# Performance work log

Measured on AMD Instinct MI355X. Metric: run time of the kernel, lower is better.

## Reference

```python
import jax, jax.numpy as jnp
import numpy as np

N_NODES = 100000


def gcn_conv(x, edge_index, W, b):
    """PyG-style GCNConv: add self-loops, symmetric deg^-1/2 normalization,
    linear transform, scatter-add aggregation."""
    n = x.shape[0]
    x = x @ W  # [N, F_out]
    # add self-loops (fixed shape -> jit friendly)
    loops = jnp.arange(n, dtype=edge_index.dtype)
    src = jnp.concatenate([edge_index[0], loops])
    dst = jnp.concatenate([edge_index[1], loops])
    # degree computed on target nodes (col), incl. self-loops
    deg = jax.ops.segment_sum(jnp.ones_like(dst, dtype=x.dtype), dst, num_segments=n)
    deg_inv_sqrt = jnp.where(deg > 0, jax.lax.rsqrt(deg), 0.0)
    norm = deg_inv_sqrt[src] * deg_inv_sqrt[dst]  # [E+N]
    msgs = x[src] * norm[:, None]  # gather + scale
    out = jax.ops.segment_sum(msgs, dst, num_segments=n)  # scatter-add
    return out + b


def setup_inputs() -> dict:
    key = jax.random.key(0)
    k1, k2, k3, k4 = jax.random.split(key, 4)
    x = jax.random.normal(k1, (N_NODES, 1), dtype=jnp.float32)
    edge_index = jax.random.randint(k2, (2, 3200000), 0, N_NODES, dtype=jnp.int64)
    W1 = jax.random.normal(k3, (1, 16), dtype=jnp.float32) * (1.0 / np.sqrt(1))
    b1 = jnp.zeros((16,), dtype=jnp.float32)
    W2 = jax.random.normal(k4, (16, 2), dtype=jnp.float32) * (1.0 / np.sqrt(16))
    b2 = jnp.zeros((2,), dtype=jnp.float32)
    return {"x": x, "edge_index": edge_index, "W1": W1, "b1": b1, "W2": W2, "b2": b2}


def reference(x, edge_index, W1, b1, W2, b2):
    h = gcn_conv(x, edge_index, W1, b1)
    h = jax.nn.relu(h)
    out = gcn_conv(h, edge_index, W2, b2)
    return out
```

## Files before the change

### kernel.cpp

```cpp
#include <hip/hip_runtime.h>

#define N_NODES 100000
#define NP 100096
#define N_EDGES 3200000
#define NB 782
#define NBP 1024
#define NHR 400
#define EPB (N_EDGES / NHR)
#define RS 10368
#define BSB 512
#define CAP 6144
#define CAPO 5120
#define CSRS 5120
#define SENT 128u

typedef unsigned char u8;

__global__ __launch_bounds__(BSB) void k_bin3(const int* __restrict__ src,
                                              const int* __restrict__ dst,
                                              unsigned* __restrict__ binned,
                                              unsigned* __restrict__ runinfoT) {
    __shared__ int hist[NBP];
    __shared__ int scanv[NBP];
    __shared__ int sh[BSB];
    __shared__ alignas(16) unsigned stage[RS];
    int t = threadIdx.x, blk = blockIdx.x;
    for (int i = t; i < NBP; i += BSB) hist[i] = 0;
    for (int i = t; i < RS; i += BSB) stage[i] = SENT;
    __syncthreads();
    int base = blk * EPB;
    for (int i = t * 4; i < EPB; i += BSB * 4) {
        int4 d = *(const int4*)(dst + base + i);
        atomicAdd(&hist[d.x >> 7], 1);
        atomicAdd(&hist[d.y >> 7], 1);
        atomicAdd(&hist[d.z >> 7], 1);
        atomicAdd(&hist[d.w >> 7], 1);
    }
    __syncthreads();
    int c0 = hist[2 * t], c1 = hist[2 * t + 1];
    int p0 = (c0 + 3) & ~3, p1 = (c1 + 3) & ~3;
    int v = p0 + p1;
    sh[t] = v;
    __syncthreads();
    for (int off = 1; off < BSB; off <<= 1) {
        int u = (t >= off) ? sh[t - off] : 0;
        __syncthreads();
        sh[t] += u;
        __syncthreads();
    }
    int excl = sh[t] - v;
    scanv[2 * t] = excl;
    scanv[2 * t + 1] = excl + p0;
    __syncthreads();
    for (int b = t; b < NB; b += BSB)
        runinfoT[(size_t)b * NHR + blk] =
            (unsigned)scanv[b] | ((unsigned)((hist[b] + 3) >> 2) << 16);
    __syncthreads();
    for (int i = t * 4; i < EPB; i += BSB * 4) {
        int4 s4 = *(const int4*)(src + base + i);
        int4 d4 = *(const int4*)(dst + base + i);
        int p;
        p = atomicAdd(&scanv[d4.x >> 7], 1);
        stage[p] = ((unsigned)s4.x << 8) | (unsigned)(d4.x & 127);
        p = atomicAdd(&scanv[d4.y >> 7], 1);
        stage[p] = ((unsigned)s4.y << 8) | (unsigned)(d4.y & 127);
        p = atomicAdd(&scanv[d4.z >> 7], 1);
        stage[p] = ((unsigned)s4.z << 8) | (unsigned)(d4.z & 127);
        p = atomicAdd(&scanv[d4.w >> 7], 1);
        stage[p] = ((unsigned)s4.w << 8) | (unsigned)(d4.w & 127);
    }
    __syncthreads();
    for (int i = t * 4; i < RS; i += BSB * 4)
        *(int4*)(binned + (size_t)blk * RS + i) = *(const int4*)(stage + i);
}

__global__ __launch_bounds__(256) void k_regroup(
        const unsigned* __restrict__ binned, const unsigned* __restrict__ runinfoT,
        const float* __restrict__ x, unsigned* __restrict__ csr,
        int* __restrict__ startv, int* __restrict__ lenv,
        float* __restrict__ dinv, float* __restrict__ s) {
    __shared__ unsigned rinfo[NHR];
    __shared__ int pref[512];
    __shared__ int sh[256];
    __shared__ alignas(16) unsigned stage[CAP];
    __shared__ unsigned outA[CAPO];
    __shared__ int cnt[128];
    __shared__ int excl[128];
    __shared__ int cur[128];
    int t = threadIdx.x, b = blockIdx.x;
    for (int r = t; r < NHR; r += 256) rinfo[r] = runinfoT[(size_t)b * NHR + r];
    if (t < 128) cnt[t] = 0;
    __syncthreads();
    int v0 = (2 * t < NHR) ? 4 * (int)(rinfo[2 * t] >> 16) : 0;
    int v1 = (2 * t + 1 < NHR) ? 4 * (int)(rinfo[2 * t + 1] >> 16) : 0;
    int vv = v0 + v1;
    sh[t] = vv;
    __syncthreads();
    for (int off = 1; off < 256; off <<= 1) {
        int u = (t >= off) ? sh[t - off] : 0;
        __syncthreads();
        sh[t] += u;
        __syncthreads();
    }
    int ex = sh[t] - vv;
    pref[2 * t] = ex;
    pref[2 * t + 1] = ex + v0;
    __syncthreads();
    int padTot = sh[255];
    int g = t >> 2, lane = t & 3;
    for (int r = g; r < NHR; r += 64) {
        unsigned ri = rinfo[r];
        int off = (int)(ri & 0xFFFFu), nq = (int)(ri >> 16);
        int bs = pref[r];
        if (bs + 4 * nq > CAP) continue;
        const uint4* p = (const uint4*)(binned + (size_t)r * RS + off);
        for (int j = lane; j < nq; j += 4) {
            uint4 w = p[j];
            *(uint4*)(&stage[bs + 4 * j]) = make_uint4(w.x, w.y, w.z, w.w);
        }
    }
    __syncthreads();
    for (int i = t; i < padTot; i += 256) {
        unsigned w = stage[i];
        if ((w & 255u) != 128u) atomicAdd(&cnt[w & 127], 1);
    }
    __syncthreads();
    if (t < 128) sh[t] = cnt[t];
    __syncthreads();
    for (int off = 1; off < 128; off <<= 1) {
        int u = (t >= off && t < 128) ? sh[t - off] : 0;
        __syncthreads();
        if (t < 128) sh[t] += u;
        __syncthreads();
    }
    if (t < 128) {
        excl[t] = sh[t] - cnt[t];
        cur[t] = sh[t] - cnt[t];
    }
    __syncthreads();
    for (int i = t; i < padTot; i += 256) {
        unsigned w = stage[i];
        if ((w & 255u) != 128u) {
            int pos = atomicAdd(&cur[w & 127], 1);
            if (pos < CAPO) outA[pos] = w >> 8;
        }
    }
    __syncthreads();
    int fillTot = excl[127] + cnt[127];
    if (fillTot > CAPO) fillTot = CAPO;
    for (int i = t; i < fillTot; i += 256)
        csr[(size_t)b * CSRS + i] = outA[i];
    if (t < 128) {
        int node = b * 128 + t;
        if (node < N_NODES) {
            int d = cnt[t];
            float di = rsqrtf((float)(d + 1));
            dinv[node] = di;
            s[node] = di * x[node];
            startv[node] = b * CSRS + excl[t];
            lenv[node] = d;
        }
    }
}

__global__ __launch_bounds__(256) void k_s1c(const unsigned* __restrict__ csr,
                                             const int* __restrict__ startv,
                                             const int* __restrict__ lenv,
                                             const float* __restrict__ dinv,
                                             const float* __restrict__ s,
                                             const float* __restrict__ W1,
                                             const float* __restrict__ b1,
                                             const float* __restrict__ W2,
                                             float2* __restrict__ z) {
    int v = blockIdx.x * 256 + threadIdx.x;
    if (v >= N_NODES) return;
    int st = startv[v], n = lenv[v];
    const unsigned* p = csr + st;
    float a0 = 0.f, a1 = 0.f, a2 = 0.f, a3 = 0.f;
    int j = 0;
    for (; j + 4 <= n; j += 4) {
        unsigned c0 = p[j], c1 = p[j + 1], c2 = p[j + 2], c3 = p[j + 3];
        float f0 = s[c0], f1 = s[c1], f2 = s[c2], f3 = s[c3];
        a0 += f0;
        a1 += f1;
        a2 += f2;
        a3 += f3;
    }
    float acc = (a0 + a1) + (a2 + a3);
    for (; j < n; ++j) acc += s[p[j]];
    float di = dinv[v];
    float a = di * (acc + s[v]);
    float z0 = 0.f, z1 = 0.f;
#pragma unroll
    for (int f = 0; f < 16; ++f) {
        float h = fmaxf(a * W1[f] + b1[f], 0.f);
        z0 += h * W2[2 * f + 0];
        z1 += h * W2[2 * f + 1];
    }
    z[v] = make_float2(di * z0, di * z1);
}

__global__ __launch_bounds__(256) void k_s2c(const unsigned* __restrict__ csr,
                                             const int* __restrict__ startv,
                                             const int* __restrict__ lenv,
                                             const float* __restrict__ dinv,
                                             const float2* __restrict__ z,
                                             const float* __restrict__ b2,
                                             float2* __restrict__ out) {
    int v = blockIdx.x * 256 + threadIdx.x;
    if (v >= N_NODES) return;
    int st = startv[v], n = lenv[v];
    const unsigned* p = csr + st;
    float x0 = 0.f, y0 = 0.f, x1 = 0.f, y1 = 0.f;
    float x2 = 0.f, y2 = 0.f, x3 = 0.f, y3 = 0.f;
    int j = 0;
    for (; j + 4 <= n; j += 4) {
        unsigned c0 = p[j], c1 = p[j + 1], c2 = p[j + 2], c3 = p[j + 3];
        float2 f0 = z[c0], f1 = z[c1], f2 = z[c2], f3 = z[c3];
        x0 += f0.x;
        y0 += f0.y;
        x1 += f1.x;
        y1 += f1.y;
        x2 += f2.x;
        y2 += f2.y;
        x3 += f3.x;
        y3 += f3.y;
    }
    float ax = (x0 + x1) + (x2 + x3);
    float ay = (y0 + y1) + (y2 + y3);
    for (; j < n; ++j) {
        float2 f = z[p[j]];
        ax += f.x;
        ay += f.y;
    }
    float2 zz = z[v];
    float di = dinv[v];
    out[v] = make_float2(di * (ax + zz.x) + b2[0], di * (ay + zz.y) + b2[1]);
}

__global__ void f_deg(const int* __restrict__ dst, int* __restrict__ deg) {
    int i = blockIdx.x * blockDim.x + threadIdx.x;
    if (i < N_EDGES) atomicAdd(&deg[dst[i]], 1);
}
__global__ void f_node1(const float* __restrict__ x, const int* __restrict__ deg,
                        float* __restrict__ dinv, float* __restrict__ s) {
    int v = blockIdx.x * blockDim.x + threadIdx.x;
    if (v < N_NODES) {
        float di = rsqrtf((float)(deg[v] + 1));
        dinv[v] = di;
        s[v] = di * x[v];
    }
}
__global__ void f_scatter1(const int* __restrict__ src, const int* __restrict__ dst,
                           const float* __restrict__ s, float* __restrict__ agg1) {
    int i = blockIdx.x * blockDim.x + threadIdx.x;
    if (i < N_EDGES) atomicAdd(&agg1[dst[i]], s[src[i]]);
}
__global__ void f_node2(const float* __restrict__ dinv, const float* __restrict__ s,
                        const float* __restrict__ agg1, const float* __restrict__ W1,
                        const float* __restrict__ b1, const float* __restrict__ W2,
                        float2* __restrict__ z) {
    int v = blockIdx.x * blockDim.x + threadIdx.x;
    if (v < N_NODES) {
        float di = dinv[v];
        float a = di * (agg1[v] + s[v]);
        float z0 = 0.f, z1 = 0.f;
#pragma unroll
        for (int f = 0; f < 16; ++f) {
            float h = fmaxf(a * W1[f] + b1[f], 0.f);
            z0 += h * W2[2 * f + 0];
            z1 += h * W2[2 * f + 1];
        }
        z[v] = make_float2(di * z0, di * z1);
    }
}
__global__ void f_scatter2(const int* __restrict__ src, const int* __restrict__ dst,
                           const float2* __restrict__ z, float* __restrict__ agg2) {
    int i = blockIdx.x * blockDim.x + threadIdx.x;
    if (i < N_EDGES) {
        float2 zz = z[src[i]];
        int d = dst[i];
        atomicAdd(&agg2[2 * d + 0], zz.x);
        atomicAdd(&agg2[2 * d + 1], zz.y);
    }
}
__global__ void f_out(const float* __restrict__ dinv, const float2* __restrict__ z,
                      const float2* __restrict__ agg2, const float* __restrict__ b2,
                      float2* __restrict__ out) {
    int v = blockIdx.x * blockDim.x + threadIdx.x;
    if (v < N_NODES) {
        float di = dinv[v];
        float2 a = agg2[v], zz = z[v];
        out[v] = make_float2(di * (a.x + zz.x) + b2[0], di * (a.y + zz.y) + b2[1]);
    }
}

extern "C" void kernel_launch(void* const* d_in, const int* in_sizes, int n_in,
                              void* d_out, int out_size, void* d_ws, size_t ws_size,
                              hipStream_t stream) {
    const float* x  = (const float*)d_in[0];
    const int* eidx = (const int*)d_in[1];
    const float* W1 = (const float*)d_in[2];
    const float* b1 = (const float*)d_in[3];
    const float* W2 = (const float*)d_in[4];
    const float* b2 = (const float*)d_in[5];
    float* out = (float*)d_out;

    const int n = N_NODES;
    const int* src = eidx;
    const int* dst = eidx + N_EDGES;

    size_t oRun   = 0;
    size_t oBin   = oRun + (size_t)NB * NHR;
    size_t oCsr   = oBin + (size_t)NHR * RS;
    size_t oStart = oCsr + (size_t)NB * CSRS;
    size_t oLen   = oStart + NP;
    size_t oDinv  = oLen + NP;
    size_t oS     = oDinv + NP;
    size_t oZ     = oS + NP;
    size_t need   = (oZ + 2 * NP) * sizeof(int);

    if (ws_size >= need) {
        int* wsI = (int*)d_ws;
        unsigned* runinfoT = (unsigned*)(wsI + oRun);
        unsigned* binned   = (unsigned*)(wsI + oBin);
        unsigned* csr      = (unsigned*)(wsI + oCsr);
        int* startv = wsI + oStart;
        int* lenv   = wsI + oLen;
        float* dinv = (float*)(wsI + oDinv);
        float* s    = (float*)(wsI + oS);
        float2* z   = (float2*)(wsI + oZ);

        k_bin3<<<NHR, BSB, 0, stream>>>(src, dst, binned, runinfoT);
        k_regroup<<<NB, 256, 0, stream>>>(binned, runinfoT, x, csr, startv, lenv,
                                          dinv, s);
        k_s1c<<<NP / 256, 256, 0, stream>>>(csr, startv, lenv, dinv, s, W1, b1,
                                            W2, z);
        k_s2c<<<NP / 256, 256, 0, stream>>>(csr, startv, lenv, dinv, z, b2,
                                            (float2*)out);
    } else {
        float* ws = (float*)d_ws;
        int* deg    = (int*)ws;
        float* agg1 = ws + n;
        float* agg2 = ws + 2 * n;
        float* dinv = ws + 4 * n;
        float* s    = ws + 5 * n;
        float* z    = ws + 6 * n;
        (void)hipMemsetAsync(d_ws, 0, (size_t)(4 * n) * sizeof(float), stream);
        const int gridE = (N_EDGES + 255) / 256;
        const int gridN = (n + 255) / 256;
        f_deg<<<gridE, 256, 0, stream>>>(dst, deg);
        f_node1<<<gridN, 256, 0, stream>>>(x, deg, dinv, s);
        f_scatter1<<<gridE, 256, 0, stream>>>(src, dst, s, agg1);
        f_node2<<<gridN, 256, 0, stream>>>(dinv, s, agg1, W1, b1, W2, (float2*)z);
        f_scatter2<<<gridE, 256, 0, stream>>>(src, dst, (const float2*)z, agg2);
        f_out<<<gridN, 256, 0, stream>>>(dinv, (const float2*)z, (const float2*)agg2,
                                         b2, (float2*)out);
    }
}
```

Measured before the change: 87.20 us.

## Pad CSR rows to 4 and gather with 4 lanes per node using uint4 loads

```diff
diff --git a/kernel.cpp b/kernel.cpp
--- a/kernel.cpp
+++ b/kernel.cpp
@@ -85,11 +85,12 @@
     __shared__ alignas(16) unsigned stage[CAP];
     __shared__ unsigned outA[CAPO];
     __shared__ int cnt[128];
-    __shared__ int excl[128];
+    __shared__ int excl4[128];
     __shared__ int cur[128];
     int t = threadIdx.x, b = blockIdx.x;
     for (int r = t; r < NHR; r += 256) rinfo[r] = runinfoT[(size_t)b * NHR + r];
     if (t < 128) cnt[t] = 0;
+    for (int i = t; i < CAPO; i += 256) outA[i] = 0xFFFFFFFFu;
     __syncthreads();
     int v0 = (2 * t < NHR) ? 4 * (int)(rinfo[2 * t] >> 16) : 0;
     int v1 = (2 * t + 1 < NHR) ? 4 * (int)(rinfo[2 * t + 1] >> 16) : 0;
@@ -125,7 +126,7 @@
         if ((w & 255u) != 128u) atomicAdd(&cnt[w & 127], 1);
     }
     __syncthreads();
-    if (t < 128) sh[t] = cnt[t];
+    if (t < 128) sh[t] = (cnt[t] + 3) & ~3;
     __syncthreads();
     for (int off = 1; off < 128; off <<= 1) {
         int u = (t >= off && t < 128) ? sh[t - off] : 0;
@@ -134,8 +135,9 @@
         __syncthreads();
     }
     if (t < 128) {
-        excl[t] = sh[t] - cnt[t];
-        cur[t] = sh[t] - cnt[t];
+        int pc = (cnt[t] + 3) & ~3;
+        excl4[t] = sh[t] - pc;
+        cur[t] = sh[t] - pc;
     }
     __syncthreads();
     for (int i = t; i < padTot; i += 256) {
@@ -146,7 +148,7 @@
         }
     }
     __syncthreads();
-    int fillTot = excl[127] + cnt[127];
+    int fillTot = excl4[127] + ((cnt[127] + 3) & ~3);
     if (fillTot > CAPO) fillTot = CAPO;
     for (int i = t; i < fillTot; i += 256)
         csr[(size_t)b * CSRS + i] = outA[i];
@@ -157,7 +159,7 @@
             float di = rsqrtf((float)(d + 1));
             dinv[node] = di;
             s[node] = di * x[node];
-            startv[node] = b * CSRS + excl[t];
+            startv[node] = b * CSRS + excl4[t];
             lenv[node] = d;
         }
     }
@@ -172,32 +174,36 @@
                                              const float* __restrict__ b1,
                                              const float* __restrict__ W2,
                                              float2* __restrict__ z) {
-    int v = blockIdx.x * 256 + threadIdx.x;
+    int t = threadIdx.x;
+    int v = blockIdx.x * 64 + (t >> 2);
+    int lane = t & 3;
     if (v >= N_NODES) return;
-    int st = startv[v], n = lenv[v];
-    const unsigned* p = csr + st;
-    float a0 = 0.f, a1 = 0.f, a2 = 0.f, a3 = 0.f;
-    int j = 0;
-    for (; j + 4 <= n; j += 4) {
-        unsigned c0 = p[j], c1 = p[j + 1], c2 = p[j + 2], c3 = p[j + 3];
-        float f0 = s[c0], f1 = s[c1], f2 = s[c2], f3 = s[c3];
-        a0 += f0;
-        a1 += f1;
-        a2 += f2;
-        a3 += f3;
-    }
-    float acc = (a0 + a1) + (a2 + a3);
-    for (; j < n; ++j) acc += s[p[j]];
-    float di = dinv[v];
-    float a = di * (acc + s[v]);
-    float z0 = 0.f, z1 = 0.f;
+    int st = startv[v], d = lenv[v];
+    int nq = (d + 3) >> 2;
+    const uint4* p = (const uint4*)(csr + st);
+    float acc = 0.f;
+    for (int j = lane; j < nq; j += 4) {
+        uint4 w = p[j];
+        float f0 = (w.x < N_NODES) ? s[w.x] : 0.f;
+        float f1 = (w.y < N_NODES) ? s[w.y] : 0.f;
+        float f2 = (w.z < N_NODES) ? s[w.z] : 0.f;
+        float f3 = (w.w < N_NODES) ? s[w.w] : 0.f;
+        acc += (f0 + f1) + (f2 + f3);
+    }
+    acc += __shfl_xor(acc, 1);
+    acc += __shfl_xor(acc, 2);
+    if (lane == 0) {
+        float di = dinv[v];
+        float a = di * (acc + s[v]);
+        float z0 = 0.f, z1 = 0.f;
 #pragma unroll
-    for (int f = 0; f < 16; ++f) {
-        float h = fmaxf(a * W1[f] + b1[f], 0.f);
-        z0 += h * W2[2 * f + 0];
-        z1 += h * W2[2 * f + 1];
-    }
-    z[v] = make_float2(di * z0, di * z1);
+        for (int f = 0; f < 16; ++f) {
+            float h = fmaxf(a * W1[f] + b1[f], 0.f);
+            z0 += h * W2[2 * f + 0];
+            z1 += h * W2[2 * f + 1];
+        }
+        z[v] = make_float2(di * z0, di * z1);
+    }
 }
 
 __global__ __launch_bounds__(256) void k_s2c(const unsigned* __restrict__ csr,
@@ -207,35 +213,30 @@
                                              const float2* __restrict__ z,
                                              const float* __restrict__ b2,
                                              float2* __restrict__ out) {
-    int v = blockIdx.x * 256 + threadIdx.x;
+    int t = threadIdx.x;
+    int v = blockIdx.x * 64 + (t >> 2);
+    int lane = t & 3;
     if (v >= N_NODES) return;
-    int st = startv[v], n = lenv[v];
-    const unsigned* p = csr + st;
-    float x0 = 0.f, y0 = 0.f, x1 = 0.f, y1 = 0.f;
-    float x2 = 0.f, y2 = 0.f, x3 = 0.f, y3 = 0.f;
-    int j = 0;
-    for (; j + 4 <= n; j += 4) {
-        unsigned c0 = p[j], c1 = p[j + 1], c2 = p[j + 2], c3 = p[j + 3];
-        float2 f0 = z[c0], f1 = z[c1], f2 = z[c2], f3 = z[c3];
-        x0 += f0.x;
-        y0 += f0.y;
-        x1 += f1.x;
-        y1 += f1.y;
-        x2 += f2.x;
-        y2 += f2.y;
-        x3 += f3.x;
-        y3 += f3.y;
-    }
-    float ax = (x0 + x1) + (x2 + x3);
-    float ay = (y0 + y1) + (y2 + y3);
-    for (; j < n; ++j) {
-        float2 f = z[p[j]];
-        ax += f.x;
-        ay += f.y;
-    }
-    float2 zz = z[v];
-    float di = dinv[v];
-    out[v] = make_float2(di * (ax + zz.x) + b2[0], di * (ay + zz.y) + b2[1]);
+    int st = startv[v], d = lenv[v];
+    int nq = (d + 3) >> 2;
+    const uint4* p = (const uint4*)(csr + st);
+    float ax = 0.f, ay = 0.f;
+    for (int j = lane; j < nq; j += 4) {
+        uint4 w = p[j];
+        if (w.x < N_NODES) { float2 f = z[w.x]; ax += f.x; ay += f.y; }
+        if (w.y < N_NODES) { float2 f = z[w.y]; ax += f.x; ay += f.y; }
+        if (w.z < N_NODES) { float2 f = z[w.z]; ax += f.x; ay += f.y; }
+        if (w.w < N_NODES) { float2 f = z[w.w]; ax += f.x; ay += f.y; }
+    }
+    ax += __shfl_xor(ax, 1);
+    ax += __shfl_xor(ax, 2);
+    ay += __shfl_xor(ay, 1);
+    ay += __shfl_xor(ay, 2);
+    if (lane == 0) {
+        float2 zz = z[v];
+        float di = dinv[v];
+        out[v] = make_float2(di * (ax + zz.x) + b2[0], di * (ay + zz.y) + b2[1]);
+    }
 }
 
 __global__ void f_deg(const int* __restrict__ dst, int* __restrict__ deg) {
@@ -331,13 +332,14 @@
         float* s    = (float*)(wsI + oS);
         float2* z   = (float2*)(wsI + oZ);
 
+        const int gridS = (N_NODES + 63) / 64;
         k_bin3<<<NHR, BSB, 0, stream>>>(src, dst, binned, runinfoT);
         k_regroup<<<NB, 256, 0, stream>>>(binned, runinfoT, x, csr, startv, lenv,
                                           dinv, s);
-        k_s1c<<<NP / 256, 256, 0, stream>>>(csr, startv, lenv, dinv, s, W1, b1,
-                                            W2, z);
-        k_s2c<<<NP / 256, 256, 0, stream>>>(csr, startv, lenv, dinv, z, b2,
-                                            (float2*)out);
+        k_s1c<<<gridS, 256, 0, stream>>>(csr, startv, lenv, dinv, s, W1, b1,
+                                         W2, z);
+        k_s2c<<<gridS, 256, 0, stream>>>(csr, startv, lenv, dinv, z, b2,
+                                         (float2*)out);
     } else {
         float* ws = (float*)d_ws;
         int* deg    = (int*)ws;
```

Measured after the change: 83.39 us. 4.4% less time.
